# Kernel optimization log

Measured on AMD Instinct MI355X. Metric: run time of the kernel, lower is better.

Reference implementation:

```python
import jax, jax.numpy as jnp
import numpy as np
from functools import partial

B, N, NCLS = 16, 25200, 80
M_TGT = 50
MAX_DET = 300
CONF_THRES = 0.8
NMS_THRES = 0.4


def cxcywh_to_xyxy(boxes):
    # cxcywh -> xywh -> xyxy (as in tensor_to_dict: cxcywh_to_xywh then xywh_to_xyxy)
    cx, cy, w, h = boxes[..., 0], boxes[..., 1], boxes[..., 2], boxes[..., 3]
    x1 = cx - 0.5 * w
    y1 = cy - 0.5 * h
    return jnp.stack([x1, y1, x1 + w, y1 + h], axis=-1)


def pairwise_iou(b):
    # b: [K,4] xyxy
    x1 = jnp.maximum(b[:, None, 0], b[None, :, 0])
    y1 = jnp.maximum(b[:, None, 1], b[None, :, 1])
    x2 = jnp.minimum(b[:, None, 2], b[None, :, 2])
    y2 = jnp.minimum(b[:, None, 3], b[None, :, 3])
    inter = jnp.clip(x2 - x1, 0.0) * jnp.clip(y2 - y1, 0.0)
    area = jnp.clip(b[:, 2] - b[:, 0], 0.0) * jnp.clip(b[:, 3] - b[:, 1], 0.0)
    return inter / (area[:, None] + area[None, :] - inter + 1e-9)


def nms_one(boxes_xyxy, labels, valid):
    # boxes sorted by score descending; class-aware greedy NMS, fixed K iterations
    K = boxes_xyxy.shape[0]
    iou = pairwise_iou(boxes_xyxy)
    same = labels[:, None] == labels[None, :]
    supp = (iou > NMS_THRES) & same
    idx = jnp.arange(K)

    def body(i, keep):
        kill = supp[i] & (idx > i) & keep[i]
        return keep & ~kill

    return jax.lax.fori_loop(0, K, body, valid)


def post_process(preds):
    # preds: [B, N, 5+C] (cx,cy,w,h,obj,cls...)
    obj = preds[..., 4]
    cls_prob = preds[..., 5:]
    cls_conf = jnp.max(cls_prob, axis=-1)
    cls_id = jnp.argmax(cls_prob, axis=-1)
    score = obj * cls_conf                      # [B,N]
    score = jnp.where(score > CONF_THRES, score, 0.0)
    top_s, top_i = jax.lax.top_k(score, MAX_DET)            # [B,K]
    boxes = jnp.take_along_axis(preds[..., :4], top_i[..., None], axis=1)  # cxcywh [B,K,4]
    labels = jnp.take_along_axis(cls_id, top_i, axis=1)     # [B,K]
    valid = top_s > 0.0
    boxes_xyxy = cxcywh_to_xyxy(boxes)
    keep = jax.vmap(nms_one)(boxes_xyxy, labels, valid)     # [B,K]
    scores = jnp.where(keep, top_s, 0.0)
    boxes_xyxy = jnp.where(keep[..., None], boxes_xyxy, 0.0)
    labels = jnp.where(keep, labels, -1)
    return boxes_xyxy, scores, labels, keep


def process_targets(tt, lengths):
    # tt: [B, M, 6] = cxcywh, score, label ; lengths: [B]
    valid = jnp.arange(tt.shape[1])[None, :] < lengths[:, None]  # [B,M]
    boxes = cxcywh_to_xyxy(tt[..., :4])
    scores = tt[..., 4]
    labels = tt[..., 5].astype(jnp.int32)
    boxes = jnp.where(valid[..., None], boxes, 0.0)
    scores = jnp.where(valid, scores, 0.0)
    labels = jnp.where(valid, labels, -1)
    return boxes, scores, labels, valid


def setup_inputs() -> dict:
    key = jax.random.key(0)
    k1, k2, k3, k4 = jax.random.split(key, 4)
    preds = jax.random.uniform(k1, (B, N, 5 + NCLS), dtype=jnp.float32)
    tgt_boxes = jax.random.uniform(k2, (B, M_TGT, 4), dtype=jnp.float32) * 640.0
    tgt_scores = jnp.ones((B, M_TGT, 1), dtype=jnp.float32)
    tgt_labels = jax.random.randint(k3, (B, M_TGT, 1), 0, NCLS).astype(jnp.float32)
    target_target = jnp.concatenate([tgt_boxes, tgt_scores, tgt_labels], axis=-1)
    target_lengths = jax.random.randint(k4, (B,), 1, M_TGT + 1).astype(jnp.int32)
    return {"preds": preds, "target_target": target_target, "target_lengths": target_lengths}


def reference(preds, target_target, target_lengths):
    pb, ps, pl, pv = post_process(preds)
    tb, ts, tl, tv = process_targets(target_target, target_lengths)
    # @torch.no_grad in original forward
    out = (pb, ps, pl, pv, tb, ts, tl, tv)
    return jax.tree_util.tree_map(jax.lax.stop_gradient, out)
```

## Files before the change

kernel.cpp:

```cpp
#include <hip/hip_runtime.h>
#include <cstdint>

#define BB 16
#define NN 25200
#define NCLS 80
#define NF (5 + NCLS)
#define MAXDET 300
#define MTGT 50
#define CONF 0.8f
#define NMSTH 0.4f
#define WORDS 10
#define NBINS 2048
#define CAPALL 8192
#define SBUF 2048
#define APB 64
#define CHUNK_V4 (APB * NF / 4)
#define SCORE_BLOCKS ((BB * NN) / APB)
#define NTGT_BLOCKS ((BB * MTGT + 127) / 128)
#define HSTRIDE 33

#define WS_SCORE 0
#define WS_DS   ((size_t)BB * NN * 4)
#define WS_DI   (WS_DS + (size_t)BB * MAXDET * 4)
#define WS_GBOX (WS_DI + (size_t)BB * MAXDET * 4)
#define WS_GLAB (WS_GBOX + (size_t)BB * MAXDET * 16)

#define O_PB 0
#define O_PS (BB * MAXDET * 4)
#define O_PL (O_PS + BB * MAXDET)
#define O_PV (O_PL + BB * MAXDET)
#define O_TB (O_PV + BB * MAXDET)
#define O_TS (O_TB + BB * MTGT * 4)
#define O_TL (O_TS + BB * MTGT)
#define O_TV (O_TL + BB * MTGT)

__global__ __launch_bounds__(128) void k_score(const float* __restrict__ preds,
                                               float* __restrict__ scores,
                                               const float* __restrict__ tt,
                                               const int* __restrict__ len,
                                               float* __restrict__ out) {
    __shared__ float st[APB * NF];
    int tid = threadIdx.x;
    int bid = blockIdx.x;

    if (bid >= SCORE_BLOCKS) {
        int t = (bid - SCORE_BLOCKS) * 128 + tid;
        if (t < BB * MTGT) {
            int b = t / MTGT, m = t - b * MTGT;
            const float* row = tt + (size_t)t * 6;
            bool valid = m < len[b];
            float cx = row[0], cy = row[1], w = row[2], h = row[3];
            float x1 = cx - 0.5f * w, y1 = cy - 0.5f * h;
            float* tb = out + O_TB + (size_t)t * 4;
            tb[0] = valid ? x1 : 0.f;
            tb[1] = valid ? y1 : 0.f;
            tb[2] = valid ? (x1 + w) : 0.f;
            tb[3] = valid ? (y1 + h) : 0.f;
            out[O_TS + t] = valid ? row[4] : 0.f;
            out[O_TL + t] = valid ? (float)(int)row[5] : -1.f;
            out[O_TV + t] = valid ? 1.f : 0.f;
        }
        return;
    }

    int w = tid >> 6;
    const float4* src = (const float4*)(preds + (size_t)bid * (APB * NF));
    #pragma unroll
    for (int i = 0; i < 11; ++i) {
        int idx = i * 128 + tid;
        if (idx < CHUNK_V4) {
            __builtin_amdgcn_global_load_lds(
                (const __attribute__((address_space(1))) void*)(src + idx),
                (__attribute__((address_space(3))) void*)(st + (i * 128 + w * 64) * 4),
                16, 0, 0);
        }
    }
    __syncthreads();

    int a = tid >> 1, h = tid & 1;
    const float* cls = st + a * NF + 5 + h * 40;
    float m0 = cls[0], m1 = cls[1], m2 = cls[2], m3 = cls[3];
    #pragma unroll
    for (int f = 4; f < 40; f += 4) {
        m0 = fmaxf(m0, cls[f]);     m1 = fmaxf(m1, cls[f + 1]);
        m2 = fmaxf(m2, cls[f + 2]); m3 = fmaxf(m3, cls[f + 3]);
    }
    float m = fmaxf(fmaxf(m0, m1), fmaxf(m2, m3));
    m = fmaxf(m, __shfl_xor(m, 1));
    if (h == 0) scores[bid * APB + a] = st[a * NF + 4] * m;
}

__global__ __launch_bounds__(1024) void k_select(const float* __restrict__ scores,
                                                 float* __restrict__ dscore,
                                                 unsigned* __restrict__ didx) {
    __shared__ unsigned long long skall[CAPALL];
    __shared__ unsigned long long sk[SBUF];
    __shared__ int hist[64 * HSTRIDE];
    __shared__ int lcnt, lcnt2, scut;
    int b = blockIdx.x;
    int tid = threadIdx.x;
    int lane = tid & 63;

    if (tid == 0) { lcnt = 0; lcnt2 = 0; }
    for (int i = tid; i < 64 * HSTRIDE; i += 1024) hist[i] = 0;
    for (int i = tid; i < SBUF; i += 1024) sk[i] = 0ull;
    __syncthreads();

    const float4* src4 = (const float4*)(scores + (size_t)b * NN);
    for (int v = tid; v < 7168; v += 1024) {
        float4 s4 = make_float4(0.f, 0.f, 0.f, 0.f);
        if (v < NN / 4) s4 = src4[v];
        #pragma unroll
        for (int c = 0; c < 4; ++c) {
            float s = (c == 0) ? s4.x : (c == 1) ? s4.y : (c == 2) ? s4.z : s4.w;
            bool pass = s > CONF;
            unsigned u = __float_as_uint(s);
            if (pass) {
                int bin = (int)((u - 0x3F400000u) >> 12);
                bin = bin < 0 ? 0 : (bin > NBINS - 1 ? NBINS - 1 : bin);
                atomicAdd(&hist[(bin >> 5) * HSTRIDE + (bin & 31)], 1);
            }
            unsigned long long mask = __ballot(pass);
            int wcnt = __popcll(mask);
            int bs = 0;
            if (lane == 0 && wcnt) bs = atomicAdd(&lcnt, wcnt);
            bs = __shfl(bs, 0);
            if (pass) {
                int pos = bs + __popcll(mask & ((1ull << lane) - 1ull));
                if (pos < CAPALL)
                    skall[pos] = ((unsigned long long)u << 32) |
                                 (unsigned long long)(0xFFFFFFFFu - (unsigned)(4 * v + c));
            }
        }
    }
    __syncthreads();

    if (tid < 64) {
        int sb = 0;
        #pragma unroll
        for (int k = 0; k < 32; ++k) sb += hist[lane * HSTRIDE + k];
        int cum = sb;
        #pragma unroll
        for (int d = 1; d < 64; d <<= 1) {
            int o = __shfl_down(cum, d);
            if (lane + d < 64) cum += o;
        }
        unsigned long long m = __ballot(cum >= MAXDET);
        int cutbin = 0;
        if (m) {
            int cutS = 63 - __clzll(m);
            int tail = (cutS < 63) ? __shfl(cum, cutS + 1) : 0;
            int hh = (lane < 32) ? hist[cutS * HSTRIDE + lane] : 0;
            int c2 = hh;
            #pragma unroll
            for (int d = 1; d < 32; d <<= 1) {
                int o = __shfl_down(c2, d);
                if (lane + d < 32) c2 += o;
            }
            c2 += tail;
            unsigned long long m2 = __ballot(lane < 32 && c2 >= MAXDET);
            int cutL = 63 - __clzll(m2);
            cutbin = cutS * 32 + cutL;
        }
        if (lane == 0) scut = cutbin;
    }
    __syncthreads();
    int cutbin = scut;

    int M = lcnt; if (M > CAPALL) M = CAPALL;
    for (int i = tid; i < ((M + 1023) & ~1023); i += 1024) {
        bool pass = false;
        unsigned long long key = 0ull;
        if (i < M) {
            key = skall[i];
            unsigned u = (unsigned)(key >> 32);
            int bin = (int)((u - 0x3F400000u) >> 12);
            bin = bin < 0 ? 0 : (bin > NBINS - 1 ? NBINS - 1 : bin);
            pass = bin >= cutbin;
        }
        unsigned long long mask = __ballot(pass);
        int wcnt = __popcll(mask);
        int bs = 0;
        if (lane == 0 && wcnt) bs = atomicAdd(&lcnt2, wcnt);
        bs = __shfl(bs, 0);
        if (pass) {
            int pos = bs + __popcll(mask & ((1ull << lane) - 1ull));
            if (pos < SBUF) sk[pos] = key;
        }
    }
    __syncthreads();

    int M2 = lcnt2; if (M2 > SBUF) M2 = SBUF;
    unsigned P = 512;
    while ((int)P < M2) P <<= 1;

    for (unsigned k = 2; k <= P; k <<= 1) {
        for (unsigned j = k >> 1; j > 0; j >>= 1) {
            __syncthreads();
            for (unsigned i = tid; i < P; i += 1024) {
                unsigned ixj = i ^ j;
                if (ixj > i) {
                    unsigned long long a = sk[i], d = sk[ixj];
                    bool desc = ((i & k) == 0);
                    if (desc ? (a < d) : (a > d)) { sk[i] = d; sk[ixj] = a; }
                }
            }
        }
    }
    __syncthreads();
    for (int q = tid; q < MAXDET; q += 1024) {
        unsigned long long key = sk[q];
        unsigned sbits = (unsigned)(key >> 32);
        dscore[b * MAXDET + q] = __uint_as_float(sbits);
        didx[b * MAXDET + q]   = sbits ? (0xFFFFFFFFu - (unsigned)(key & 0xFFFFFFFFu)) : 0u;
    }
}

__global__ __launch_bounds__(512) void k_gather(const float* __restrict__ preds,
                                                const float* __restrict__ dscore,
                                                const unsigned* __restrict__ didx,
                                                float* __restrict__ gbox,
                                                int* __restrict__ glabel) {
    int g    = blockIdx.x * 8 + (threadIdx.x >> 6);
    int lane = threadIdx.x & 63;
    float sc = dscore[g];
    if (sc > 0.f) {
        int b = g / MAXDET;
        int idx = (int)didx[g];
        const float* row = preds + ((size_t)b * NN + (size_t)idx) * NF;
        float v = row[5 + lane]; int ci = lane;
        if (lane < 16) { float v2 = row[69 + lane]; if (v2 > v) { v = v2; ci = lane + 64; } }
        #pragma unroll
        for (int m = 32; m >= 1; m >>= 1) {
            float ov = __shfl_xor(v, m);
            int   oi = __shfl_xor(ci, m);
            if (ov > v || (ov == v && oi < ci)) { v = ov; ci = oi; }
        }
        if (lane == 0) {
            float cx = row[0], cy = row[1], w = row[2], h = row[3];
            float x1 = cx - 0.5f * w, y1 = cy - 0.5f * h;
            float4 bx = { x1, y1, x1 + w, y1 + h };
            ((float4*)gbox)[g] = bx;
            glabel[g] = ci;
        }
    } else if (lane == 0) {
        float4 zz = { 0.f, 0.f, 0.f, 0.f };
        ((float4*)gbox)[g] = zz;
        glabel[g] = -1;
    }
}

__global__ __launch_bounds__(1024) void k_nms2(const float* __restrict__ gbox,
                                               const int* __restrict__ glabel,
                                               const float* __restrict__ dscore,
                                               float* __restrict__ out) {
    __shared__ float4   sbox[MAXDET];
    __shared__ int      slabel[MAXDET];
    __shared__ float    sscore[MAXDET];
    __shared__ unsigned supp[MAXDET * WORDS];
    int b = blockIdx.x;
    int tid = threadIdx.x;

    if (tid < MAXDET) {
        int g = b * MAXDET + tid;
        sbox[tid]   = ((const float4*)gbox)[g];
        slabel[tid] = glabel[g];
        sscore[tid] = dscore[g];
    }
    __syncthreads();

    for (int T = tid; T < MAXDET * WORDS; T += 1024) {
        int i  = T / WORDS;
        int jw = T - i * WORDS;
        unsigned word = 0;
        int jbase = jw * 32;
        if (jbase + 31 > i) {
            float4 bi = sbox[i];
            int   li = slabel[i];
            float si = sscore[i];
            float ai = __fmul_rn(fmaxf(__fsub_rn(bi.z, bi.x), 0.f),
                                 fmaxf(__fsub_rn(bi.w, bi.y), 0.f));
            for (int uu = 0; uu < 32; ++uu) {
                int t = (uu + jw) & 31;
                int j = jbase + t;
                if (j > i && j < MAXDET) {
                    if (slabel[j] == li && si > 0.f && sscore[j] > 0.f) {
                        float4 bj = sbox[j];
                        float xx1 = fmaxf(bi.x, bj.x);
                        float yy1 = fmaxf(bi.y, bj.y);
                        float xx2 = fminf(bi.z, bj.z);
                        float yy2 = fminf(bi.w, bj.w);
                        float iw = fmaxf(__fsub_rn(xx2, xx1), 0.f);
                        float ih = fmaxf(__fsub_rn(yy2, yy1), 0.f);
                        float inter = __fmul_rn(iw, ih);
                        float aj = __fmul_rn(fmaxf(__fsub_rn(bj.z, bj.x), 0.f),
                                             fmaxf(__fsub_rn(bj.w, bj.y), 0.f));
                        float den = __fadd_rn(__fsub_rn(__fadd_rn(ai, aj), inter), 1e-9f);
                        float iou = inter / den;
                        if (iou > NMSTH) word |= 1u << t;
                    }
                }
            }
        }
        supp[T] = word;
    }
    __syncthreads();

    if (tid < 64) {
        int lane = tid;
        unsigned keep = 0, nzm = 0;
        #pragma unroll
        for (int s = 0; s < 5; ++s) {
            int k = s * 64 + lane;
            bool kb = (k < MAXDET) && (sscore[k] > 0.f);
            unsigned long long m = __ballot(kb);
            if (lane == 2 * s)     keep = (unsigned)m;
            if (lane == 2 * s + 1) keep = (unsigned)(m >> 32);
            unsigned nz = 0;
            if (k < MAXDET) {
                #pragma unroll
                for (int w = 0; w < WORDS; ++w) nz |= supp[k * WORDS + w];
            }
            unsigned long long mn = __ballot(nz != 0u);
            if (lane == 2 * s)     nzm = (unsigned)mn;
            if (lane == 2 * s + 1) nzm = (unsigned)(mn >> 32);
        }

        for (int i = 0; i < MAXDET; ++i) {
            int idx = i >> 5;
            unsigned kw = __shfl(keep, idx);
            unsigned nw = __shfl(nzm, idx);
            if (((kw & nw) >> (i & 31)) & 1u) {
                if (lane < WORDS) keep &= ~supp[i * WORDS + lane];
            }
        }

        #pragma unroll
        for (int s = 0; s < 5; ++s) {
            int k = s * 64 + lane;
            if (k < MAXDET) {
                unsigned kw = __shfl(keep, k >> 5);
                bool kp = (kw >> (k & 31)) & 1u;
                int g = b * MAXDET + k;
                float4 bx = sbox[k];
                float4 zz = { 0.f, 0.f, 0.f, 0.f };
                ((float4*)(out + O_PB))[g] = kp ? bx : zz;
                out[O_PS + g] = kp ? sscore[k] : 0.f;
                out[O_PL + g] = kp ? (float)slabel[k] : -1.f;
                out[O_PV + g] = kp ? 1.f : 0.f;
            }
        }
    }
}

extern "C" void kernel_launch(void* const* d_in, const int* in_sizes, int n_in,
                              void* d_out, int out_size, void* d_ws, size_t ws_size,
                              hipStream_t stream) {
    const float* preds = (const float*)d_in[0];
    const float* tt    = (const float*)d_in[1];
    const int*   len   = (const int*)d_in[2];
    float* out = (float*)d_out;

    char* ws = (char*)d_ws;
    float*    scores = (float*)(ws + WS_SCORE);
    float*    dscore = (float*)(ws + WS_DS);
    unsigned* didx   = (unsigned*)(ws + WS_DI);
    float*    gbox   = (float*)(ws + WS_GBOX);
    int*      glabel = (int*)(ws + WS_GLAB);

    k_score <<<SCORE_BLOCKS + NTGT_BLOCKS, 128, 0, stream>>>(preds, scores, tt, len, out);
    k_select<<<BB, 1024, 0, stream>>>(scores, dscore, didx);
    k_gather<<<(BB * MAXDET) / 8, 512, 0, stream>>>(preds, dscore, didx, gbox, glabel);
    k_nms2  <<<BB, 1024, 0, stream>>>(gbox, glabel, dscore, out);
}
```

Before: 89.07 us.

## Fuse threshold filtering and histogram into score kernel via global atomics

The score kernel now applies the confidence threshold itself, bins passing scores into a per-batch global histogram, and compacts passing keys into a per-batch global buffer. This replaces the full dense score array and the select kernel's scan over all 25200 scores per image. The block mapping is changed so that chunks do not straddle images. It adds a zeroing kernel launch and global atomics, and the select kernel now reads the histogram and keys from global memory.

Result: slower. 122.7 us (+37.7%).

```diff
diff --git a/kernel.cpp b/kernel.cpp
--- a/kernel.cpp
+++ b/kernel.cpp
@@ -11,16 +11,18 @@
 #define NMSTH 0.4f
 #define WORDS 10
 #define NBINS 2048
-#define CAPALL 8192
 #define SBUF 2048
+#define CAPK 8192
 #define APB 64
-#define CHUNK_V4 (APB * NF / 4)
-#define SCORE_BLOCKS ((BB * NN) / APB)
+#define CPB 394
+#define SCORE_BLOCKS (BB * CPB)
 #define NTGT_BLOCKS ((BB * MTGT + 127) / 128)
 #define HSTRIDE 33
 
-#define WS_SCORE 0
-#define WS_DS   ((size_t)BB * NN * 4)
+#define WS_HIST 0
+#define WS_CNT  (131072)
+#define WS_KEYS (WS_CNT + 1024)
+#define WS_DS   (WS_KEYS + (size_t)BB * CAPK * 8)
 #define WS_DI   (WS_DS + (size_t)BB * MAXDET * 4)
 #define WS_GBOX (WS_DI + (size_t)BB * MAXDET * 4)
 #define WS_GLAB (WS_GBOX + (size_t)BB * MAXDET * 16)
@@ -34,8 +36,17 @@
 #define O_TL (O_TS + BB * MTGT)
 #define O_TV (O_TL + BB * MTGT)
 
+__global__ __launch_bounds__(1024) void k_zero(int* __restrict__ ghist,
+                                               int* __restrict__ cnt) {
+    int i = blockIdx.x * 1024 + threadIdx.x;
+    if (i < BB * NBINS) ghist[i] = 0;
+    if (i < 256) cnt[i] = 0;
+}
+
 __global__ __launch_bounds__(128) void k_score(const float* __restrict__ preds,
-                                               float* __restrict__ scores,
+                                               int* __restrict__ ghist,
+                                               int* __restrict__ cnt,
+                                               unsigned long long* __restrict__ keys,
                                                const float* __restrict__ tt,
                                                const int* __restrict__ len,
                                                float* __restrict__ out) {
@@ -63,12 +74,17 @@
         return;
     }
 
+    int b  = bid / CPB;
+    int cb = bid - b * CPB;
+    int count = (cb == CPB - 1) ? (NN - (CPB - 1) * APB) : APB;
+    int nv4 = count * NF / 4;
+
     int w = tid >> 6;
-    const float4* src = (const float4*)(preds + (size_t)bid * (APB * NF));
+    const float4* src = (const float4*)(preds + ((size_t)b * NN + (size_t)cb * APB) * NF);
     #pragma unroll
     for (int i = 0; i < 11; ++i) {
         int idx = i * 128 + tid;
-        if (idx < CHUNK_V4) {
+        if (idx < nv4) {
             __builtin_amdgcn_global_load_lds(
                 (const __attribute__((address_space(1))) void*)(src + idx),
                 (__attribute__((address_space(3))) void*)(st + (i * 128 + w * 64) * 4),
@@ -78,61 +94,61 @@
     __syncthreads();
 
     int a = tid >> 1, h = tid & 1;
-    const float* cls = st + a * NF + 5 + h * 40;
-    float m0 = cls[0], m1 = cls[1], m2 = cls[2], m3 = cls[3];
-    #pragma unroll
-    for (int f = 4; f < 40; f += 4) {
-        m0 = fmaxf(m0, cls[f]);     m1 = fmaxf(m1, cls[f + 1]);
-        m2 = fmaxf(m2, cls[f + 2]); m3 = fmaxf(m3, cls[f + 3]);
-    }
-    float m = fmaxf(fmaxf(m0, m1), fmaxf(m2, m3));
-    m = fmaxf(m, __shfl_xor(m, 1));
-    if (h == 0) scores[bid * APB + a] = st[a * NF + 4] * m;
-}
-
-__global__ __launch_bounds__(1024) void k_select(const float* __restrict__ scores,
+    bool pass = false;
+    unsigned long long key = 0ull;
+    if (a < count) {
+        const float* cls = st + a * NF + 5 + h * 40;
+        float m0 = cls[0], m1 = cls[1], m2 = cls[2], m3 = cls[3];
+        #pragma unroll
+        for (int f = 4; f < 40; f += 4) {
+            m0 = fmaxf(m0, cls[f]);     m1 = fmaxf(m1, cls[f + 1]);
+            m2 = fmaxf(m2, cls[f + 2]); m3 = fmaxf(m3, cls[f + 3]);
+        }
+        float m = fmaxf(fmaxf(m0, m1), fmaxf(m2, m3));
+        m = fmaxf(m, __shfl_xor(m, 1));
+        if (h == 0) {
+            float s = st[a * NF + 4] * m;
+            if (s > CONF) {
+                pass = true;
+                unsigned u = __float_as_uint(s);
+                int bin = (int)((u - 0x3F400000u) >> 12);
+                bin = bin < 0 ? 0 : (bin > NBINS - 1 ? NBINS - 1 : bin);
+                atomicAdd(&ghist[b * NBINS + bin], 1);
+                unsigned aidx = (unsigned)(cb * APB + a);
+                key = ((unsigned long long)u << 32) |
+                      (unsigned long long)(0xFFFFFFFFu - aidx);
+            }
+        }
+    }
+    int lane = tid & 63;
+    unsigned long long mask = __ballot(pass);
+    int wcnt = __popcll(mask);
+    int bs = 0;
+    if (lane == 0 && wcnt) bs = atomicAdd(&cnt[b * 16], wcnt);
+    bs = __shfl(bs, 0);
+    if (pass) {
+        int pos = bs + __popcll(mask & ((1ull << lane) - 1ull));
+        if (pos < CAPK) keys[(size_t)b * CAPK + pos] = key;
+    }
+}
+
+__global__ __launch_bounds__(1024) void k_select(const int* __restrict__ ghist,
+                                                 const int* __restrict__ cnt,
+                                                 const unsigned long long* __restrict__ keys,
                                                  float* __restrict__ dscore,
                                                  unsigned* __restrict__ didx) {
-    __shared__ unsigned long long skall[CAPALL];
+    __shared__ int hist[64 * HSTRIDE];
     __shared__ unsigned long long sk[SBUF];
-    __shared__ int hist[64 * HSTRIDE];
-    __shared__ int lcnt, lcnt2, scut;
+    __shared__ int lcnt2;
+    __shared__ int scut;
     int b = blockIdx.x;
     int tid = threadIdx.x;
     int lane = tid & 63;
 
-    if (tid == 0) { lcnt = 0; lcnt2 = 0; }
-    for (int i = tid; i < 64 * HSTRIDE; i += 1024) hist[i] = 0;
+    if (tid == 0) lcnt2 = 0;
     for (int i = tid; i < SBUF; i += 1024) sk[i] = 0ull;
-    __syncthreads();
-
-    const float4* src4 = (const float4*)(scores + (size_t)b * NN);
-    for (int v = tid; v < 7168; v += 1024) {
-        float4 s4 = make_float4(0.f, 0.f, 0.f, 0.f);
-        if (v < NN / 4) s4 = src4[v];
-        #pragma unroll
-        for (int c = 0; c < 4; ++c) {
-            float s = (c == 0) ? s4.x : (c == 1) ? s4.y : (c == 2) ? s4.z : s4.w;
-            bool pass = s > CONF;
-            unsigned u = __float_as_uint(s);
-            if (pass) {
-                int bin = (int)((u - 0x3F400000u) >> 12);
-                bin = bin < 0 ? 0 : (bin > NBINS - 1 ? NBINS - 1 : bin);
-                atomicAdd(&hist[(bin >> 5) * HSTRIDE + (bin & 31)], 1);
-            }
-            unsigned long long mask = __ballot(pass);
-            int wcnt = __popcll(mask);
-            int bs = 0;
-            if (lane == 0 && wcnt) bs = atomicAdd(&lcnt, wcnt);
-            bs = __shfl(bs, 0);
-            if (pass) {
-                int pos = bs + __popcll(mask & ((1ull << lane) - 1ull));
-                if (pos < CAPALL)
-                    skall[pos] = ((unsigned long long)u << 32) |
-                                 (unsigned long long)(0xFFFFFFFFu - (unsigned)(4 * v + c));
-            }
-        }
-    }
+    for (int i = tid; i < NBINS; i += 1024)
+        hist[(i >> 5) * HSTRIDE + (i & 31)] = ghist[b * NBINS + i];
     __syncthreads();
 
     if (tid < 64) {
@@ -167,12 +183,12 @@
     __syncthreads();
     int cutbin = scut;
 
-    int M = lcnt; if (M > CAPALL) M = CAPALL;
+    int M = cnt[b * 16]; if (M > CAPK) M = CAPK;
     for (int i = tid; i < ((M + 1023) & ~1023); i += 1024) {
         bool pass = false;
         unsigned long long key = 0ull;
         if (i < M) {
-            key = skall[i];
+            key = keys[(size_t)b * CAPK + i];
             unsigned u = (unsigned)(key >> 32);
             int bin = (int)((u - 0x3F400000u) >> 12);
             bin = bin < 0 ? 0 : (bin > NBINS - 1 ? NBINS - 1 : bin);
@@ -362,14 +378,17 @@
     float* out = (float*)d_out;
 
     char* ws = (char*)d_ws;
-    float*    scores = (float*)(ws + WS_SCORE);
+    int*      ghist  = (int*)(ws + WS_HIST);
+    int*      cnt    = (int*)(ws + WS_CNT);
+    unsigned long long* keys = (unsigned long long*)(ws + WS_KEYS);
     float*    dscore = (float*)(ws + WS_DS);
     unsigned* didx   = (unsigned*)(ws + WS_DI);
     float*    gbox   = (float*)(ws + WS_GBOX);
     int*      glabel = (int*)(ws + WS_GLAB);
 
-    k_score <<<SCORE_BLOCKS + NTGT_BLOCKS, 128, 0, stream>>>(preds, scores, tt, len, out);
-    k_select<<<BB, 1024, 0, stream>>>(scores, dscore, didx);
+    k_zero  <<<(BB * NBINS + 1023) / 1024, 1024, 0, stream>>>(ghist, cnt);
+    k_score <<<SCORE_BLOCKS + NTGT_BLOCKS, 128, 0, stream>>>(preds, ghist, cnt, keys, tt, len, out);
+    k_select<<<BB, 1024, 0, stream>>>(ghist, cnt, keys, dscore, didx);
     k_gather<<<(BB * MAXDET) / 8, 512, 0, stream>>>(preds, dscore, didx, gbox, glabel);
     k_nms2  <<<BB, 1024, 0, stream>>>(gbox, glabel, dscore, out);
 }
```

## Fuse top-k selection, gather and NMS into one per-image kernel

Applied to the files above, without the earlier changes.

Merges the select, gather and NMS kernels into a single per-batch kernel. Sorted keys now stay in shared memory, boxes and labels are gathered straight into shared arrays, and NMS runs in the same block. This removes two kernel launches and the workspace round trips. In exchange, the gather uses only 600 threads per block, each scanning 40 class scores serially, where the old kernel used a wide 64-lane gather grid. Shared memory per block also grows.

Result: no change. 88.21 us (-1.0%).

```diff
diff --git a/kernel.cpp b/kernel.cpp
--- a/kernel.cpp
+++ b/kernel.cpp
@@ -20,10 +20,6 @@
 #define HSTRIDE 33
 
 #define WS_SCORE 0
-#define WS_DS   ((size_t)BB * NN * 4)
-#define WS_DI   (WS_DS + (size_t)BB * MAXDET * 4)
-#define WS_GBOX (WS_DI + (size_t)BB * MAXDET * 4)
-#define WS_GLAB (WS_GBOX + (size_t)BB * MAXDET * 16)
 
 #define O_PB 0
 #define O_PS (BB * MAXDET * 4)
@@ -90,12 +86,16 @@
     if (h == 0) scores[bid * APB + a] = st[a * NF + 4] * m;
 }
 
-__global__ __launch_bounds__(1024) void k_select(const float* __restrict__ scores,
-                                                 float* __restrict__ dscore,
-                                                 unsigned* __restrict__ didx) {
+__global__ __launch_bounds__(1024) void k_post(const float* __restrict__ scores,
+                                               const float* __restrict__ preds,
+                                               float* __restrict__ out) {
     __shared__ unsigned long long skall[CAPALL];
     __shared__ unsigned long long sk[SBUF];
     __shared__ int hist[64 * HSTRIDE];
+    __shared__ float4   sbox[MAXDET];
+    __shared__ int      slabel[MAXDET];
+    __shared__ float    sscore[MAXDET];
+    __shared__ unsigned supp[MAXDET * WORDS];
     __shared__ int lcnt, lcnt2, scut;
     int b = blockIdx.x;
     int tid = threadIdx.x;
@@ -193,7 +193,6 @@
     int M2 = lcnt2; if (M2 > SBUF) M2 = SBUF;
     unsigned P = 512;
     while ((int)P < M2) P <<= 1;
-
     for (unsigned k = 2; k <= P; k <<= 1) {
         for (unsigned j = k >> 1; j > 0; j >>= 1) {
             __syncthreads();
@@ -208,64 +207,38 @@
         }
     }
     __syncthreads();
-    for (int q = tid; q < MAXDET; q += 1024) {
-        unsigned long long key = sk[q];
-        unsigned sbits = (unsigned)(key >> 32);
-        dscore[b * MAXDET + q] = __uint_as_float(sbits);
-        didx[b * MAXDET + q]   = sbits ? (0xFFFFFFFFu - (unsigned)(key & 0xFFFFFFFFu)) : 0u;
-    }
-}
-
-__global__ __launch_bounds__(512) void k_gather(const float* __restrict__ preds,
-                                                const float* __restrict__ dscore,
-                                                const unsigned* __restrict__ didx,
-                                                float* __restrict__ gbox,
-                                                int* __restrict__ glabel) {
-    int g    = blockIdx.x * 8 + (threadIdx.x >> 6);
-    int lane = threadIdx.x & 63;
-    float sc = dscore[g];
-    if (sc > 0.f) {
-        int b = g / MAXDET;
-        int idx = (int)didx[g];
-        const float* row = preds + ((size_t)b * NN + (size_t)idx) * NF;
-        float v = row[5 + lane]; int ci = lane;
-        if (lane < 16) { float v2 = row[69 + lane]; if (v2 > v) { v = v2; ci = lane + 64; } }
-        #pragma unroll
-        for (int m = 32; m >= 1; m >>= 1) {
-            float ov = __shfl_xor(v, m);
-            int   oi = __shfl_xor(ci, m);
-            if (ov > v || (ov == v && oi < ci)) { v = ov; ci = oi; }
-        }
-        if (lane == 0) {
-            float cx = row[0], cy = row[1], w = row[2], h = row[3];
-            float x1 = cx - 0.5f * w, y1 = cy - 0.5f * h;
-            float4 bx = { x1, y1, x1 + w, y1 + h };
-            ((float4*)gbox)[g] = bx;
-            glabel[g] = ci;
-        }
-    } else if (lane == 0) {
-        float4 zz = { 0.f, 0.f, 0.f, 0.f };
-        ((float4*)gbox)[g] = zz;
-        glabel[g] = -1;
-    }
-}
-
-__global__ __launch_bounds__(1024) void k_nms2(const float* __restrict__ gbox,
-                                               const int* __restrict__ glabel,
-                                               const float* __restrict__ dscore,
-                                               float* __restrict__ out) {
-    __shared__ float4   sbox[MAXDET];
-    __shared__ int      slabel[MAXDET];
-    __shared__ float    sscore[MAXDET];
-    __shared__ unsigned supp[MAXDET * WORDS];
-    int b = blockIdx.x;
-    int tid = threadIdx.x;
-
-    if (tid < MAXDET) {
-        int g = b * MAXDET + tid;
-        sbox[tid]   = ((const float4*)gbox)[g];
-        slabel[tid] = glabel[g];
-        sscore[tid] = dscore[g];
+
+    {
+        int k = tid >> 1, h = tid & 1;
+        if (k < MAXDET) {
+            unsigned long long key = sk[k];
+            unsigned sbits = (unsigned)(key >> 32);
+            if (sbits) {
+                int idx = (int)(0xFFFFFFFFu - (unsigned)(key & 0xFFFFFFFFu));
+                const float* row = preds + ((size_t)b * NN + (size_t)idx) * NF;
+                const float* cls = row + 5 + h * 40;
+                float v = cls[0]; int ci = h * 40;
+                #pragma unroll
+                for (int f = 1; f < 40; ++f) {
+                    float x = cls[f];
+                    if (x > v) { v = x; ci = h * 40 + f; }
+                }
+                float ov = __shfl_xor(v, 1);
+                int   oi = __shfl_xor(ci, 1);
+                if (ov > v || (ov == v && oi < ci)) { v = ov; ci = oi; }
+                if (h == 0) {
+                    float cx = row[0], cy = row[1], w = row[2], hh = row[3];
+                    float x1 = cx - 0.5f * w, y1 = cy - 0.5f * hh;
+                    float4 bx = { x1, y1, x1 + w, y1 + hh };
+                    sbox[k] = bx;
+                    slabel[k] = ci;
+                    sscore[k] = __uint_as_float(sbits);
+                }
+            } else if (h == 0) {
+                float4 zz = { 0.f, 0.f, 0.f, 0.f };
+                sbox[k] = zz; slabel[k] = -1; sscore[k] = 0.f;
+            }
+        }
     }
     __syncthreads();
 
@@ -307,7 +280,6 @@
     __syncthreads();
 
     if (tid < 64) {
-        int lane = tid;
         unsigned keep = 0, nzm = 0;
         #pragma unroll
         for (int s = 0; s < 5; ++s) {
@@ -361,15 +333,8 @@
     const int*   len   = (const int*)d_in[2];
     float* out = (float*)d_out;
 
-    char* ws = (char*)d_ws;
-    float*    scores = (float*)(ws + WS_SCORE);
-    float*    dscore = (float*)(ws + WS_DS);
-    unsigned* didx   = (unsigned*)(ws + WS_DI);
-    float*    gbox   = (float*)(ws + WS_GBOX);
-    int*      glabel = (int*)(ws + WS_GLAB);
-
-    k_score <<<SCORE_BLOCKS + NTGT_BLOCKS, 128, 0, stream>>>(preds, scores, tt, len, out);
-    k_select<<<BB, 1024, 0, stream>>>(scores, dscore, didx);
-    k_gather<<<(BB * MAXDET) / 8, 512, 0, stream>>>(preds, dscore, didx, gbox, glabel);
-    k_nms2  <<<BB, 1024, 0, stream>>>(gbox, glabel, dscore, out);
+    float* scores = (float*)((char*)d_ws + WS_SCORE);
+
+    k_score<<<SCORE_BLOCKS + NTGT_BLOCKS, 128, 0, stream>>>(preds, scores, tt, len, out);
+    k_post <<<BB, 1024, 0, stream>>>(scores, preds, out);
 }
```
